# Performance work log

Hardware: AMD Instinct MI355X
Metric: run time of the kernel (lower is better)

The kernel has to match this reference:

```python
import jax, jax.numpy as jnp
import numpy as np

B, S, D, H = 2, 2048, 1024, 16
HD = D // H  # head dim = 64


def setup_inputs() -> dict:
    key = jax.random.key(0)
    ks = jax.random.split(key, 8)
    s = 0.02
    return {
        "Q": jax.random.normal(ks[0], (B, S, D), jnp.float32),
        "K": jax.random.normal(ks[1], (B, S, D), jnp.float32),
        "V": jax.random.normal(ks[2], (B, S, D), jnp.float32),
        "mask": jax.random.randint(ks[3], (1, 1, S, S), 0, 2, jnp.int32),
        "Wq": jax.random.normal(ks[4], (D, D), jnp.float32) * s,
        "bq": jnp.zeros((D,), jnp.float32),
        "Wk": jax.random.normal(ks[5], (D, D), jnp.float32) * s,
        "bk": jnp.zeros((D,), jnp.float32),
        "Wv": jax.random.normal(ks[6], (D, D), jnp.float32) * s,
        "bv": jnp.zeros((D,), jnp.float32),
        "Wo": jax.random.normal(ks[7], (D, D), jnp.float32) * s,
        "bo": jnp.zeros((D,), jnp.float32),
    }


def reference(Q, K, V, mask, Wq, bq, Wk, bk, Wv, bv, Wo, bo):
    b = Q.shape[0]
    # QKV projections, split into heads: [B,S,D] -> [B,H,S,HD]
    q = (Q @ Wq + bq).reshape(b, -1, H, HD).transpose(0, 2, 1, 3)
    k = (K @ Wk + bk).reshape(b, -1, H, HD).transpose(0, 2, 1, 3)
    v = (V @ Wv + bv).reshape(b, -1, H, HD).transpose(0, 2, 1, 3)
    # scaled dot-product attention with full [B,H,S,S] scores (as in source)
    scale = jnp.sqrt(jnp.asarray(HD, q.dtype))
    scores = jnp.einsum("bhqd,bhkd->bhqk", q, k) / scale
    scores = jnp.where(mask == 0, -jnp.inf, scores)
    attn = jax.nn.softmax(scores, axis=-1)
    ctx = jnp.einsum("bhqk,bhkd->bhqd", attn, v)
    # merge heads and output projection
    concat = ctx.transpose(0, 2, 1, 3).reshape(b, -1, H * HD)
    return concat @ Wo + bo
```

## Files before the change

kernel.cpp:

```cpp
#include <hip/hip_runtime.h>


using s8v = __attribute__((ext_vector_type(8))) short;
using f4v = __attribute__((ext_vector_type(4))) float;
using f16v = __attribute__((ext_vector_type(16))) float;
typedef unsigned long long u64;

__device__ __forceinline__ unsigned short f2bf(float f) {
  union { float f; unsigned int u; } v; v.f = f;
  return (unsigned short)((v.u + 0x7fffu + ((v.u >> 16) & 1u)) >> 16);
}

__device__ __forceinline__ unsigned pkbf(float lo, float hi2) {
  return __builtin_amdgcn_perm(__float_as_uint(hi2), __float_as_uint(lo), 0x07060302);
}

__device__ __forceinline__ void gll16(const void* g, void* l) {
  __builtin_amdgcn_global_load_lds(
      (const __attribute__((address_space(1))) unsigned int*)g,
      (__attribute__((address_space(3))) unsigned int*)l, 16, 0, 0);
}

__global__ void prep_kernel(const float* __restrict__ Q, const float* __restrict__ K,
                            const float* __restrict__ V,
                            unsigned short* __restrict__ qb, unsigned short* __restrict__ kb,
                            unsigned short* __restrict__ vb,
                            const float* __restrict__ W0, const float* __restrict__ W1,
                            const float* __restrict__ W2, const float* __restrict__ W3,
                            unsigned short* __restrict__ T0, unsigned short* __restrict__ T1,
                            unsigned short* __restrict__ T2, unsigned short* __restrict__ T3,
                            const int* __restrict__ mask, unsigned* __restrict__ bmw) {
  __shared__ unsigned short t[64][72];
  const int bid = blockIdx.x, tid = threadIdx.x;
  if (bid < 12288) {
    int z = bid >> 12;
    int idx = (bid & 4095) * 256 + tid;
    const float* in = (z == 0) ? Q : (z == 1) ? K : V;
    unsigned short* out = (z == 0) ? qb : (z == 1) ? kb : vb;
    float4 v = ((const float4*)in)[idx];
    ushort4 o;
    o.x = f2bf(v.x); o.y = f2bf(v.y); o.z = f2bf(v.z); o.w = f2bf(v.w);
    ((ushort4*)out)[idx] = o;
  } else if (bid < 13312) {
    int b = bid - 12288;
    int z = b >> 8, rem = b & 255;
    int k0 = (rem >> 4) * 64, n0 = (rem & 15) * 64;
    const float* W = (z == 0) ? W0 : (z == 1) ? W1 : (z == 2) ? W2 : W3;
    unsigned short* Wt = (z == 0) ? T0 : (z == 1) ? T1 : (z == 2) ? T2 : T3;
    for (int p = 0; p < 4; ++p) {
      int idx = p * 256 + tid;
      int row = idx >> 4, c4 = idx & 15;
      float4 v = *(const float4*)&W[(size_t)(k0 + row) * 1024 + n0 + c4 * 4];
      t[row][c4 * 4 + 0] = f2bf(v.x);
      t[row][c4 * 4 + 1] = f2bf(v.y);
      t[row][c4 * 4 + 2] = f2bf(v.z);
      t[row][c4 * 4 + 3] = f2bf(v.w);
    }
    __syncthreads();
    for (int p = 0; p < 2; ++p) {
      int idx = p * 256 + tid;
      int j = idx >> 3, c8 = idx & 7;
      unsigned short tmp[8];
      for (int i = 0; i < 8; ++i) tmp[i] = t[c8 * 8 + i][j];
      uint4 o;
      o.x = tmp[0] | ((unsigned)tmp[1] << 16);
      o.y = tmp[2] | ((unsigned)tmp[3] << 16);
      o.z = tmp[4] | ((unsigned)tmp[5] << 16);
      o.w = tmp[6] | ((unsigned)tmp[7] << 16);
      *(uint4*)&Wt[(size_t)(n0 + j) * 1024 + k0 + c8 * 8] = o;
    }
  } else {
    int g = (bid - 13312) * 256 + tid;
    int widx = g & 15, hi = (g >> 4) & 1, l31 = (g >> 5) & 31;
    int it = (g >> 10) & 31, rowblk = g >> 15;
    int ni = widx >> 3, kcl = (widx >> 2) & 1, e = widx & 3;
    int kk = 64 * it + 32 * ni + 16 * kcl + 4 * hi + (e >> 1) * 8 + (e & 1) * 2;
    int qrow = rowblk * 32 + l31;
    const int* mrow = mask + (size_t)qrow * 2048 + kk;
    unsigned wd = (mrow[0] ? 0xFFFFu : 0u) | (mrow[1] ? 0xFFFF0000u : 0u);
    bmw[g] = wd;
  }
}

__global__ __launch_bounds__(256) void proj3_kernel(
    const unsigned short* __restrict__ A0, const unsigned short* __restrict__ A1,
    const unsigned short* __restrict__ A2,
    const unsigned short* __restrict__ W0, const unsigned short* __restrict__ W1,
    const unsigned short* __restrict__ W2,
    const float* __restrict__ b0, const float* __restrict__ b1, const float* __restrict__ b2,
    unsigned short* __restrict__ oq, unsigned short* __restrict__ ok,
    unsigned short* __restrict__ ovt) {
  const int z = blockIdx.z;
  const unsigned short* A  = (z == 0) ? A0 : (z == 1) ? A1 : A2;
  const unsigned short* Wt = (z == 0) ? W0 : (z == 1) ? W1 : W2;
  const float* bias        = (z == 0) ? b0 : (z == 1) ? b1 : b2;

  __shared__ __align__(16) union SH {
    struct { unsigned short As[2][4096]; unsigned short Bs[2][4096]; } kb;
    unsigned short Ls[128][136];
  } sh;

  const int tid = threadIdx.x;
  const int lane = tid & 63, w = tid >> 6, ln = lane & 15, quad = lane >> 4;
  const int wm = (w & 1) * 64, wn = (w >> 1) * 64;
  const int m0 = blockIdx.x * 128, n0 = blockIdx.y * 128;

  const int slr = lane >> 2;
  const int schunk = (lane & 3) ^ ((lane >> 3) & 3);
  const int cfrag = (quad ^ ((ln >> 1) & 3)) * 8;

  auto STAGE = [&](int buf, int kt) {
    gll16(&A[(size_t)(m0 + w * 32 + slr) * 1024 + kt + schunk * 8],       &sh.kb.As[buf][(w * 32) * 32]);
    gll16(&A[(size_t)(m0 + w * 32 + 16 + slr) * 1024 + kt + schunk * 8],  &sh.kb.As[buf][(w * 32 + 16) * 32]);
    gll16(&Wt[(size_t)(n0 + w * 32 + slr) * 1024 + kt + schunk * 8],      &sh.kb.Bs[buf][(w * 32) * 32]);
    gll16(&Wt[(size_t)(n0 + w * 32 + 16 + slr) * 1024 + kt + schunk * 8], &sh.kb.Bs[buf][(w * 32 + 16) * 32]);
  };

  f4v zero = {0.f, 0.f, 0.f, 0.f};
  f4v acc[4][4];
  for (int mi = 0; mi < 4; ++mi)
    for (int ni = 0; ni < 4; ++ni) acc[mi][ni] = zero;

  STAGE(0, 0);
  __syncthreads();

  for (int kt = 0; kt < 1024; kt += 32) {
    const int cur = (kt >> 5) & 1;
    if (kt + 32 < 1024) STAGE(cur ^ 1, kt + 32);
    s8v a[4], b[4];
    for (int mi = 0; mi < 4; ++mi) a[mi] = *(const s8v*)&sh.kb.As[cur][(wm + mi * 16 + ln) * 32 + cfrag];
    for (int ni = 0; ni < 4; ++ni) b[ni] = *(const s8v*)&sh.kb.Bs[cur][(wn + ni * 16 + ln) * 32 + cfrag];
    if (z < 2) {
      for (int mi = 0; mi < 4; ++mi)
        for (int ni = 0; ni < 4; ++ni)
          acc[mi][ni] = __builtin_amdgcn_mfma_f32_16x16x32_bf16(a[mi], b[ni], acc[mi][ni], 0, 0, 0);
    } else {
      for (int mi = 0; mi < 4; ++mi)
        for (int ni = 0; ni < 4; ++ni)
          acc[mi][ni] = __builtin_amdgcn_mfma_f32_16x16x32_bf16(b[ni], a[mi], acc[mi][ni], 0, 0, 0);
    }
    __syncthreads();
  }

  if (z < 2) {
    const float qscale = (z == 0) ? 0.18033688f : 1.0f;
    for (int mi = 0; mi < 4; ++mi) {
      int row = wm + mi * 16 + quad * 4;
      for (int ni = 0; ni < 4; ++ni) {
        int col = wn + ni * 16 + ln;
        float bvv = bias[n0 + col];
        for (int r = 0; r < 4; ++r)
          sh.Ls[row + r][col] = f2bf((acc[mi][ni][r] + bvv) * qscale);
      }
    }
  } else {
    for (int ni = 0; ni < 4; ++ni) {
      for (int r = 0; r < 4; ++r) {
        int colw = wn + ni * 16 + quad * 4 + r;
        float bvv = bias[n0 + colw];
        for (int mi = 0; mi < 4; ++mi) {
          int rowg = wm + mi * 16 + ln;
          sh.Ls[colw][rowg] = f2bf(acc[mi][ni][r] + bvv);
        }
      }
    }
  }
  __syncthreads();

  if (z < 2) {
    unsigned short* outp = (z == 0) ? oq : ok;
    for (int p = 0; p < 8; ++p) {
      int row = p * 16 + (tid >> 4);
      int cg  = tid & 15;
      uint4 vv = *(const uint4*)&sh.Ls[row][cg * 8];
      int rb = m0 + row, b_ = rb >> 11, s = rb & 2047;
      int colg = n0 + cg * 8, h = colg >> 6, hd = colg & 63;
      *(uint4*)&outp[(((size_t)(b_ * 16 + h)) * 2048 + s) * 64 + hd] = vv;
    }
  } else {
    for (int p = 0; p < 8; ++p) {
      int rr = p * 16 + (tid >> 4);
      int cg = tid & 15;
      uint4 vv = *(const uint4*)&sh.Ls[rr][cg * 8];
      int colw = n0 + rr, h = colw >> 6, hd = colw & 63;
      int sg = m0 + cg * 8, b_ = sg >> 11, ss = sg & 2047;
      *(uint4*)&ovt[(((size_t)(b_ * 16 + h)) * 64 + hd) * 2048 + ss] = vv;
    }
  }
}

#define FLASH_ITER(i, SIN0, SIN1, SOUT0, SOUT1)                                 \
  {                                                                             \
    const int cur = (i) & 1;                                                    \
    uint4 nA, nB, nC, nD;                                                       \
    if ((i) < 31) {                                                             \
      const uint4* m4 = (const uint4*)(mwp + ((i) + 1) * 1024);                 \
      nA = m4[0]; nB = m4[1]; nC = m4[2]; nD = m4[3];                           \
    }                                                                           \
          \
    __builtin_amdgcn_s_setprio(1);                                              \
    if ((i) < 31) {                                                             \
      s8v ak0 = *(const s8v*)&k_s[cur ^ 1][l31][hi * 8];                        \
      s8v ak1 = *(const s8v*)&k_s[cur ^ 1][32 + l31][hi * 8];                   \
      SOUT0 = __builtin_amdgcn_mfma_f32_32x32x16_bf16(ak0, qf[0], zf, 0, 0, 0); \
      SOUT1 = __builtin_amdgcn_mfma_f32_32x32x16_bf16(ak1, qf[0], zf, 0, 0, 0); \
      _Pragma("unroll")                                                         \
      for (int c = 1; c < 4; ++c) {                                             \
        ak0 = *(const s8v*)&k_s[cur ^ 1][l31][c * 16 + hi * 8];                 \
        ak1 = *(const s8v*)&k_s[cur ^ 1][32 + l31][c * 16 + hi * 8];            \
        SOUT0 = __builtin_amdgcn_mfma_f32_32x32x16_bf16(ak0, qf[c], SOUT0, 0, 0, 0); \
        SOUT1 = __builtin_amdgcn_mfma_f32_32x32x16_bf16(ak1, qf[c], SOUT1, 0, 0, 0); \
      }                                                                         \
    }                                                                           \
    __builtin_amdgcn_s_setprio(0);                                              \
         \
    s8v pf[4];                                                                  \
    _Pragma("unroll")                                                           \
    for (int ni = 0; ni < 2; ++ni) {                                            \
      const f16v sv = ni ? SIN1 : SIN0;                                         \
      _Pragma("unroll")                                                         \
      for (int kcl = 0; kcl < 2; ++kcl) {                                       \
        const int rb = 8 * kcl;                                                 \
        const uint4 mw = ni ? (kcl ? mwD : mwC) : (kcl ? mwB : mwA);            \
        unsigned x0 = pkbf(__builtin_amdgcn_exp2f(sv[rb + 0]),                  \
                           __builtin_amdgcn_exp2f(sv[rb + 1])) & mw.x;          \
        unsigned x1 = pkbf(__builtin_amdgcn_exp2f(sv[rb + 2]),                  \
                           __builtin_amdgcn_exp2f(sv[rb + 3])) & mw.y;          \
        unsigned y0 = pkbf(__builtin_amdgcn_exp2f(sv[rb + 4]),                  \
                           __builtin_amdgcn_exp2f(sv[rb + 5])) & mw.z;          \
        unsigned y1 = pkbf(__builtin_amdgcn_exp2f(sv[rb + 6]),                  \
                           __builtin_amdgcn_exp2f(sv[rb + 7])) & mw.w;          \
        asm("v_permlane32_swap_b32 %0, %1" : "+v"(x0), "+v"(y0));               \
        asm("v_permlane32_swap_b32 %0, %1" : "+v"(x1), "+v"(y1));               \
        union { uint4 u; s8v v; } cv;                                           \
        cv.u = make_uint4(x0, x1, y0, y1);                                      \
        pf[ni * 2 + kcl] = cv.v;                                                \
      }                                                                         \
    }                                                                           \
                                              \
    __builtin_amdgcn_s_setprio(1);                                              \
    _Pragma("unroll")                                                           \
    for (int kc = 0; kc < 4; ++kc)                                              \
      lac = __builtin_amdgcn_mfma_f32_32x32x16_bf16(pf[kc], ones, lac, 0, 0, 0);\
    _Pragma("unroll")                                                           \
    for (int kc = 0; kc < 4; ++kc) {                                            \
      s8v bv0 = *(const s8v*)&v_s[cur][l31][kc * 16 + hi * 8];                  \
      s8v bv1 = *(const s8v*)&v_s[cur][32 + l31][kc * 16 + hi * 8];             \
      o0 = __builtin_amdgcn_mfma_f32_32x32x16_bf16(pf[kc], bv0, o0, 0, 0, 0);   \
      o1 = __builtin_amdgcn_mfma_f32_32x32x16_bf16(pf[kc], bv1, o1, 0, 0, 0);   \
    }                                                                           \
    __builtin_amdgcn_s_setprio(0);                                              \
    __syncthreads();                             \
    if ((i) < 30) WRITET(cur);                         \
    if ((i) < 29) LOADT((i) + 3);                                               \
    __syncthreads();                      \
    mwA = nA; mwB = nB; mwC = nC; mwD = nD;                                     \
  }

__global__ __launch_bounds__(256, 2) void flash_kernel(
    const unsigned short* __restrict__ q, const unsigned short* __restrict__ k,
    const unsigned short* __restrict__ vt, const unsigned* __restrict__ bmw,
    unsigned short* __restrict__ ctx) {
  __shared__ __align__(16) unsigned short k_s[2][64][72];
  __shared__ __align__(16) unsigned short v_s[2][64][72];

  const int tid = threadIdx.x;
  const int lane = tid & 63, w = tid >> 6;
  const int l31 = lane & 31, hi = lane >> 5;
  const int q0 = blockIdx.x * 128;
  const int bh = blockIdx.y;
  const unsigned short* qg  = q  + ((size_t)bh * 2048 + q0) * 64;
  const unsigned short* kgb = k  + (size_t)bh * 2048 * 64;
  const unsigned short* vgb = vt + (size_t)bh * 64 * 2048;
  const unsigned* mwp = bmw + (size_t)(blockIdx.x * 4 + w) * 32768 + l31 * 32 + hi * 16;

  const int qrow = w * 32 + l31;
  s8v qf[4];
#pragma unroll
  for (int c = 0; c < 4; ++c)
    qf[c] = *(const s8v*)&qg[(size_t)qrow * 64 + c * 16 + hi * 8];

  s8v ones;
#pragma unroll
  for (int i = 0; i < 8; ++i) ones[i] = (short)0x3F80;
  f16v zf;
#pragma unroll
  for (int i = 0; i < 16; ++i) zf[i] = 0.f;

  const int srow = tid >> 3, sc8 = tid & 7;

  uint4 kr0, kr1, vr0, vr1;
  auto LOADT = [&](int it) {
    const int kk = it * 64;
    kr0 = *(const uint4*)&kgb[(size_t)(kk + srow) * 64 + sc8 * 8];
    kr1 = *(const uint4*)&kgb[(size_t)(kk + srow + 32) * 64 + sc8 * 8];
    vr0 = *(const uint4*)&vgb[(size_t)srow * 2048 + kk + sc8 * 8];
    vr1 = *(const uint4*)&vgb[(size_t)(srow + 32) * 2048 + kk + sc8 * 8];
  };
  auto WRITET = [&](int b) {
    *(uint4*)&k_s[b][srow][sc8 * 8] = kr0;
    *(uint4*)&k_s[b][srow + 32][sc8 * 8] = kr1;
    *(uint4*)&v_s[b][srow][sc8 * 8] = vr0;
    *(uint4*)&v_s[b][srow + 32][sc8 * 8] = vr1;
  };

  LOADT(0); WRITET(0);
  LOADT(1); WRITET(1);
  LOADT(2);
  __syncthreads();

  uint4 mwA, mwB, mwC, mwD;
  {
    const uint4* m4 = (const uint4*)mwp;
    mwA = m4[0]; mwB = m4[1]; mwC = m4[2]; mwD = m4[3];
  }

  f16v sA0, sA1, sB0, sB1;
  {
    s8v ak0 = *(const s8v*)&k_s[0][l31][hi * 8];
    s8v ak1 = *(const s8v*)&k_s[0][32 + l31][hi * 8];
    sA0 = __builtin_amdgcn_mfma_f32_32x32x16_bf16(ak0, qf[0], zf, 0, 0, 0);
    sA1 = __builtin_amdgcn_mfma_f32_32x32x16_bf16(ak1, qf[0], zf, 0, 0, 0);
#pragma unroll
    for (int c = 1; c < 4; ++c) {
      ak0 = *(const s8v*)&k_s[0][l31][c * 16 + hi * 8];
      ak1 = *(const s8v*)&k_s[0][32 + l31][c * 16 + hi * 8];
      sA0 = __builtin_amdgcn_mfma_f32_32x32x16_bf16(ak0, qf[c], sA0, 0, 0, 0);
      sA1 = __builtin_amdgcn_mfma_f32_32x32x16_bf16(ak1, qf[c], sA1, 0, 0, 0);
    }
  }

  f16v o0, o1, lac;
#pragma unroll
  for (int i = 0; i < 16; ++i) { o0[i] = 0.f; o1[i] = 0.f; lac[i] = 0.f; }

  for (int ii = 0; ii < 16; ++ii) {
    const int i0 = ii * 2;
    FLASH_ITER(i0,     sA0, sA1, sB0, sB1);
    FLASH_ITER(i0 + 1, sB0, sB1, sA0, sA1);
  }

  const int b_ = bh >> 4, h = bh & 15;
#pragma unroll
  for (int r = 0; r < 16; ++r) {
    const int ql = (r & 3) + 8 * (r >> 2) + 4 * hi;
    const float inv = 1.f / lac[r];
    const int srw = q0 + w * 32 + ql;
    const size_t base = ((size_t)b_ * 2048 + srw) * 1024 + h * 64;
    ctx[base + l31] = f2bf(o0[r] * inv);
    ctx[base + 32 + l31] = f2bf(o1[r] * inv);
  }
}

__global__ __launch_bounds__(256) void gemm_out_kernel(
    const unsigned short* __restrict__ A, const unsigned short* __restrict__ Wt,
    const float* __restrict__ bias, float* __restrict__ out) {
  __shared__ __align__(16) unsigned short As[2][4096];
  __shared__ __align__(16) unsigned short Bs[2][4096];

  const int tid = threadIdx.x;
  const int lane = tid & 63, w = tid >> 6, ln = lane & 15, quad = lane >> 4;
  const int wm = (w & 1) * 64, wn = (w >> 1) * 64;
  const int m0 = blockIdx.x * 128, n0 = blockIdx.y * 128;

  const int slr = lane >> 2;
  const int schunk = (lane & 3) ^ ((lane >> 3) & 3);
  const int cfrag = (quad ^ ((ln >> 1) & 3)) * 8;

  auto STAGE = [&](int buf, int kt) {
    gll16(&A[(size_t)(m0 + w * 32 + slr) * 1024 + kt + schunk * 8],       &As[buf][(w * 32) * 32]);
    gll16(&A[(size_t)(m0 + w * 32 + 16 + slr) * 1024 + kt + schunk * 8],  &As[buf][(w * 32 + 16) * 32]);
    gll16(&Wt[(size_t)(n0 + w * 32 + slr) * 1024 + kt + schunk * 8],      &Bs[buf][(w * 32) * 32]);
    gll16(&Wt[(size_t)(n0 + w * 32 + 16 + slr) * 1024 + kt + schunk * 8], &Bs[buf][(w * 32 + 16) * 32]);
  };

  f4v zero = {0.f, 0.f, 0.f, 0.f};
  f4v acc[4][4];
  for (int mi = 0; mi < 4; ++mi)
    for (int ni = 0; ni < 4; ++ni) acc[mi][ni] = zero;

  STAGE(0, 0);
  __syncthreads();

  for (int kt = 0; kt < 1024; kt += 32) {
    const int cur = (kt >> 5) & 1;
    if (kt + 32 < 1024) STAGE(cur ^ 1, kt + 32);
    s8v a[4], b[4];
    for (int mi = 0; mi < 4; ++mi) a[mi] = *(const s8v*)&As[cur][(wm + mi * 16 + ln) * 32 + cfrag];
    for (int ni = 0; ni < 4; ++ni) b[ni] = *(const s8v*)&Bs[cur][(wn + ni * 16 + ln) * 32 + cfrag];
    for (int mi = 0; mi < 4; ++mi)
      for (int ni = 0; ni < 4; ++ni)
        acc[mi][ni] = __builtin_amdgcn_mfma_f32_16x16x32_bf16(a[mi], b[ni], acc[mi][ni], 0, 0, 0);
    __syncthreads();
  }

  for (int mi = 0; mi < 4; ++mi) {
    int rb = m0 + wm + mi * 16 + quad * 4;
    for (int ni = 0; ni < 4; ++ni) {
      int col = n0 + wn + ni * 16 + ln;
      float bvv = bias[col];
      for (int r = 0; r < 4; ++r)
        out[(size_t)(rb + r) * 1024 + col] = acc[mi][ni][r] + bvv;
    }
  }
}

extern "C" void kernel_launch(void* const* d_in, const int* in_sizes, int n_in,
                              void* d_out, int out_size, void* d_ws, size_t ws_size,
                              hipStream_t stream) {
  const float* Q  = (const float*)d_in[0];
  const float* K  = (const float*)d_in[1];
  const float* V  = (const float*)d_in[2];
  const int* mask = (const int*)d_in[3];
  const float* Wq = (const float*)d_in[4];
  const float* bq = (const float*)d_in[5];
  const float* Wk = (const float*)d_in[6];
  const float* bk = (const float*)d_in[7];
  const float* Wv = (const float*)d_in[8];
  const float* bv = (const float*)d_in[9];
  const float* Wo = (const float*)d_in[10];
  const float* bo = (const float*)d_in[11];
  float* out = (float*)d_out;

  char* ws = (char*)d_ws;
  const size_t MB = 1u << 20;
  unsigned short* qb  = (unsigned short*)(ws + 0 * MB);
  unsigned short* kb  = (unsigned short*)(ws + 8 * MB);
  unsigned short* vb  = (unsigned short*)(ws + 16 * MB);
  unsigned short* wqt = (unsigned short*)(ws + 24 * MB);
  unsigned short* wkt = (unsigned short*)(ws + 26 * MB);
  unsigned short* wvt = (unsigned short*)(ws + 28 * MB);
  unsigned short* wot = (unsigned short*)(ws + 30 * MB);
  unsigned short* qh  = (unsigned short*)(ws + 32 * MB);
  unsigned short* kh  = (unsigned short*)(ws + 40 * MB);
  unsigned short* vth = (unsigned short*)(ws + 48 * MB);
  unsigned* bmw       = (unsigned*)(ws + 56 * MB);
  unsigned short* ctx = (unsigned short*)(ws + 16 * MB);

  prep_kernel<<<21504, 256, 0, stream>>>(Q, K, V, qb, kb, vb,
                                         Wq, Wk, Wv, Wo, wqt, wkt, wvt, wot,
                                         mask, bmw);
  proj3_kernel<<<dim3(32, 8, 3), 256, 0, stream>>>(qb, kb, vb, wqt, wkt, wvt,
                                                   bq, bk, bv, qh, kh, vth);
  flash_kernel<<<dim3(16, 32), 256, 0, stream>>>(qh, kh, vth, bmw, ctx);
  gemm_out_kernel<<<dim3(32, 8), 256, 0, stream>>>(ctx, wot, bo, out);
}
```

Measured before the change: 247.3 us.

## Triple-buffer GEMM K-loop with counted waits and halve output GEMM M-tile

Both the QKV projection kernel and the output projection kernel now use a three-stage LDS ring with two tiles in flight, waiting with explicit vmcnt counts and raw barriers instead of a full __syncthreads per step. This lets global-to-LDS loads overlap more with MFMA work. The output GEMM also drops to 64-row tiles, doubling its grid to 512 blocks for better CU occupancy on the 256-CU part, at the cost of less reuse of the weight tile. The hand-counted waits depend on the exact number of loads per stage and are fragile.

New measurement: 242.5 us. No clear change (-2.0%).

```diff
diff --git a/kernel.cpp b/kernel.cpp
--- a/kernel.cpp
+++ b/kernel.cpp
@@ -96,7 +96,7 @@
   const float* bias        = (z == 0) ? b0 : (z == 1) ? b1 : b2;
 
   __shared__ __align__(16) union SH {
-    struct { unsigned short As[2][4096]; unsigned short Bs[2][4096]; } kb;
+    unsigned short KB[3][8192];
     unsigned short Ls[128][136];
   } sh;
 
@@ -110,10 +110,10 @@
   const int cfrag = (quad ^ ((ln >> 1) & 3)) * 8;
 
   auto STAGE = [&](int buf, int kt) {
-    gll16(&A[(size_t)(m0 + w * 32 + slr) * 1024 + kt + schunk * 8],       &sh.kb.As[buf][(w * 32) * 32]);
-    gll16(&A[(size_t)(m0 + w * 32 + 16 + slr) * 1024 + kt + schunk * 8],  &sh.kb.As[buf][(w * 32 + 16) * 32]);
-    gll16(&Wt[(size_t)(n0 + w * 32 + slr) * 1024 + kt + schunk * 8],      &sh.kb.Bs[buf][(w * 32) * 32]);
-    gll16(&Wt[(size_t)(n0 + w * 32 + 16 + slr) * 1024 + kt + schunk * 8], &sh.kb.Bs[buf][(w * 32 + 16) * 32]);
+    gll16(&A[(size_t)(m0 + w * 32 + slr) * 1024 + kt + schunk * 8],       &sh.KB[buf][(w * 32) * 32]);
+    gll16(&A[(size_t)(m0 + w * 32 + 16 + slr) * 1024 + kt + schunk * 8],  &sh.KB[buf][(w * 32 + 16) * 32]);
+    gll16(&Wt[(size_t)(n0 + w * 32 + slr) * 1024 + kt + schunk * 8],      &sh.KB[buf][4096 + (w * 32) * 32]);
+    gll16(&Wt[(size_t)(n0 + w * 32 + 16 + slr) * 1024 + kt + schunk * 8], &sh.KB[buf][4096 + (w * 32 + 16) * 32]);
   };
 
   f4v zero = {0.f, 0.f, 0.f, 0.f};
@@ -122,14 +122,22 @@
     for (int ni = 0; ni < 4; ++ni) acc[mi][ni] = zero;
 
   STAGE(0, 0);
-  __syncthreads();
-
-  for (int kt = 0; kt < 1024; kt += 32) {
-    const int cur = (kt >> 5) & 1;
-    if (kt + 32 < 1024) STAGE(cur ^ 1, kt + 32);
+  STAGE(1, 32);
+  asm volatile("s_waitcnt vmcnt(4)" ::: "memory");
+  __builtin_amdgcn_s_barrier();
+  __builtin_amdgcn_sched_barrier(0);
+
+  int cur = 0;
+  for (int step = 0; step < 32; ++step) {
+    if (step < 30) {
+      const int nb = (cur == 0) ? 2 : cur - 1;
+      STAGE(nb, step * 32 + 64);
+    }
+    const unsigned short* Asb = &sh.KB[cur][0];
+    const unsigned short* Bsb = &sh.KB[cur][4096];
     s8v a[4], b[4];
-    for (int mi = 0; mi < 4; ++mi) a[mi] = *(const s8v*)&sh.kb.As[cur][(wm + mi * 16 + ln) * 32 + cfrag];
-    for (int ni = 0; ni < 4; ++ni) b[ni] = *(const s8v*)&sh.kb.Bs[cur][(wn + ni * 16 + ln) * 32 + cfrag];
+    for (int mi = 0; mi < 4; ++mi) a[mi] = *(const s8v*)&Asb[(wm + mi * 16 + ln) * 32 + cfrag];
+    for (int ni = 0; ni < 4; ++ni) b[ni] = *(const s8v*)&Bsb[(wn + ni * 16 + ln) * 32 + cfrag];
     if (z < 2) {
       for (int mi = 0; mi < 4; ++mi)
         for (int ni = 0; ni < 4; ++ni)
@@ -139,8 +147,15 @@
         for (int ni = 0; ni < 4; ++ni)
           acc[mi][ni] = __builtin_amdgcn_mfma_f32_16x16x32_bf16(b[ni], a[mi], acc[mi][ni], 0, 0, 0);
     }
-    __syncthreads();
-  }
+    if (step < 30)       asm volatile("s_waitcnt vmcnt(4)" ::: "memory");
+    else if (step == 30) asm volatile("s_waitcnt vmcnt(0)" ::: "memory");
+    if (step < 31) {
+      __builtin_amdgcn_s_barrier();
+      __builtin_amdgcn_sched_barrier(0);
+    }
+    cur = (cur == 2) ? 0 : cur + 1;
+  }
+  __syncthreads();
 
   if (z < 2) {
     const float qscale = (z == 0) ? 0.18033688f : 1.0f;
@@ -355,46 +370,57 @@
 __global__ __launch_bounds__(256) void gemm_out_kernel(
     const unsigned short* __restrict__ A, const unsigned short* __restrict__ Wt,
     const float* __restrict__ bias, float* __restrict__ out) {
-  __shared__ __align__(16) unsigned short As[2][4096];
-  __shared__ __align__(16) unsigned short Bs[2][4096];
+  __shared__ __align__(16) unsigned short As[3][2048];
+  __shared__ __align__(16) unsigned short Bs[3][4096];
 
   const int tid = threadIdx.x;
   const int lane = tid & 63, w = tid >> 6, ln = lane & 15, quad = lane >> 4;
-  const int wm = (w & 1) * 64, wn = (w >> 1) * 64;
-  const int m0 = blockIdx.x * 128, n0 = blockIdx.y * 128;
+  const int wm = (w & 1) * 32, wn = (w >> 1) * 64;
+  const int m0 = blockIdx.x * 64, n0 = blockIdx.y * 128;
 
   const int slr = lane >> 2;
   const int schunk = (lane & 3) ^ ((lane >> 3) & 3);
   const int cfrag = (quad ^ ((ln >> 1) & 3)) * 8;
 
   auto STAGE = [&](int buf, int kt) {
-    gll16(&A[(size_t)(m0 + w * 32 + slr) * 1024 + kt + schunk * 8],       &As[buf][(w * 32) * 32]);
-    gll16(&A[(size_t)(m0 + w * 32 + 16 + slr) * 1024 + kt + schunk * 8],  &As[buf][(w * 32 + 16) * 32]);
+    gll16(&A[(size_t)(m0 + w * 16 + slr) * 1024 + kt + schunk * 8],       &As[buf][(w * 16) * 32]);
     gll16(&Wt[(size_t)(n0 + w * 32 + slr) * 1024 + kt + schunk * 8],      &Bs[buf][(w * 32) * 32]);
     gll16(&Wt[(size_t)(n0 + w * 32 + 16 + slr) * 1024 + kt + schunk * 8], &Bs[buf][(w * 32 + 16) * 32]);
   };
 
   f4v zero = {0.f, 0.f, 0.f, 0.f};
-  f4v acc[4][4];
-  for (int mi = 0; mi < 4; ++mi)
+  f4v acc[2][4];
+  for (int mi = 0; mi < 2; ++mi)
     for (int ni = 0; ni < 4; ++ni) acc[mi][ni] = zero;
 
   STAGE(0, 0);
-  __syncthreads();
-
-  for (int kt = 0; kt < 1024; kt += 32) {
-    const int cur = (kt >> 5) & 1;
-    if (kt + 32 < 1024) STAGE(cur ^ 1, kt + 32);
-    s8v a[4], b[4];
-    for (int mi = 0; mi < 4; ++mi) a[mi] = *(const s8v*)&As[cur][(wm + mi * 16 + ln) * 32 + cfrag];
+  STAGE(1, 32);
+  asm volatile("s_waitcnt vmcnt(3)" ::: "memory");
+  __builtin_amdgcn_s_barrier();
+  __builtin_amdgcn_sched_barrier(0);
+
+  int cur = 0;
+  for (int step = 0; step < 32; ++step) {
+    if (step < 30) {
+      const int nb = (cur == 0) ? 2 : cur - 1;
+      STAGE(nb, step * 32 + 64);
+    }
+    s8v a[2], b[4];
+    for (int mi = 0; mi < 2; ++mi) a[mi] = *(const s8v*)&As[cur][(wm + mi * 16 + ln) * 32 + cfrag];
     for (int ni = 0; ni < 4; ++ni) b[ni] = *(const s8v*)&Bs[cur][(wn + ni * 16 + ln) * 32 + cfrag];
-    for (int mi = 0; mi < 4; ++mi)
+    for (int mi = 0; mi < 2; ++mi)
       for (int ni = 0; ni < 4; ++ni)
         acc[mi][ni] = __builtin_amdgcn_mfma_f32_16x16x32_bf16(a[mi], b[ni], acc[mi][ni], 0, 0, 0);
-    __syncthreads();
-  }
-
-  for (int mi = 0; mi < 4; ++mi) {
+    if (step < 30)       asm volatile("s_waitcnt vmcnt(3)" ::: "memory");
+    else if (step == 30) asm volatile("s_waitcnt vmcnt(0)" ::: "memory");
+    if (step < 31) {
+      __builtin_amdgcn_s_barrier();
+      __builtin_amdgcn_sched_barrier(0);
+    }
+    cur = (cur == 2) ? 0 : cur + 1;
+  }
+
+  for (int mi = 0; mi < 2; ++mi) {
     int rb = m0 + wm + mi * 16 + quad * 4;
     for (int ni = 0; ni < 4; ++ni) {
       int col = n0 + wn + ni * 16 + ln;
@@ -443,5 +469,5 @@
   proj3_kernel<<<dim3(32, 8, 3), 256, 0, stream>>>(qb, kb, vb, wqt, wkt, wvt,
                                                    bq, bk, bv, qh, kh, vth);
   flash_kernel<<<dim3(16, 32), 256, 0, stream>>>(qh, kh, vth, bmw, ctx);
-  gemm_out_kernel<<<dim3(32, 8), 256, 0, stream>>>(ctx, wot, bo, out);
-}
+  gemm_out_kernel<<<dim3(64, 8), 256, 0, stream>>>(ctx, wot, bo, out);
+}
```
